# Kernel tuning notes

Hardware: AMD Instinct MI355X
Metric: run time of the kernel (lower is better)

The kernel has to match this reference:

```python
import jax, jax.numpy as jnp
import numpy as np

B, D, S, F, C, H, OUT = 4, 60, 512, 158, 64, 128, 1
LN_EPS = 1e-5


def setup_inputs() -> dict:
    key = jax.random.key(0)
    ks = jax.random.split(key, 12)
    g = lambda k, shape, s=0.05: jax.random.normal(k, shape, dtype=jnp.float32) * s
    return dict(
        x=jax.random.normal(ks[0], (B, D, S, F), dtype=jnp.float32),
        feature_mask=jax.random.randint(ks[1], (B, D, S), 0, 2).astype(bool),
        wq=g(ks[2], (F, C)), bq=jnp.zeros((C,), jnp.float32),
        wk=g(ks[3], (F, C)), bk=jnp.zeros((C,), jnp.float32),
        wv=g(ks[4], (F, C)), bv=jnp.zeros((C,), jnp.float32),
        ln_g=jnp.ones((F + C,), jnp.float32), ln_b=jnp.zeros((F + C,), jnp.float32),
        w_ih=g(ks[5], (3 * H, F + C)), w_hh=g(ks[6], (3 * H, H)),
        b_ih=jnp.zeros((3 * H,), jnp.float32), b_hh=jnp.zeros((3 * H,), jnp.float32),
        w1=g(ks[7], (H, H // 2)), b1=jnp.zeros((H // 2,), jnp.float32),
        w2=g(ks[8], (H // 2, OUT)), b2=jnp.zeros((OUT,), jnp.float32),
    )


def reference(x, feature_mask, wq, bq, wk, bk, wv, bv, ln_g, ln_b,
              w_ih, w_hh, b_ih, b_hh, w1, b1, w2, b2):
    b, d, s, f = x.shape
    c = wq.shape[1]
    h_dim = w_hh.shape[1]

    # --- market context attention, vectorized over (batch, days) ---
    Q = x @ wq + bq            # (B,D,S,C)
    K = x @ wk + bk
    V = x @ wv + bv
    scores = jnp.einsum('bdsc,bdtc->bdst', Q, K) / jnp.sqrt(jnp.float32(c))
    scores = jnp.where(feature_mask[:, :, None, :], scores, -1e9)  # mask keys
    attn = jax.nn.softmax(scores, axis=-1)
    ctx = jnp.einsum('bdst,bdtc->bdsc', attn, V)       # (B,D,S,C)
    ctx = jnp.where(feature_mask[..., None], ctx, 0.0)  # mask queries
    denom = jnp.maximum(feature_mask.sum(axis=2), 1).astype(x.dtype)  # (B,D)
    market = ctx.sum(axis=2) / denom[..., None]         # (B,D,C)

    # --- concat + layernorm ---
    aug = jnp.concatenate(
        [x, jnp.broadcast_to(market[:, :, None, :], (b, d, s, c))], axis=-1)
    mu = aug.mean(-1, keepdims=True)
    var = aug.var(-1, keepdims=True)
    aug = (aug - mu) / jnp.sqrt(var + LN_EPS) * ln_g + ln_b  # (B,D,S,F+C)

    # --- GRU over days, batch = B*S independent sequences ---
    seq = aug.transpose(1, 0, 2, 3).reshape(d, b * s, f + c)  # (D, N, F+C)
    x_proj = seq @ w_ih.T + b_ih                               # (D, N, 3H)

    def step(h, xp):
        hp = h @ w_hh.T + b_hh
        xr, xz, xn = jnp.split(xp, 3, axis=-1)
        hr, hz, hn = jnp.split(hp, 3, axis=-1)
        r = jax.nn.sigmoid(xr + hr)
        z = jax.nn.sigmoid(xz + hz)
        n = jnp.tanh(xn + r * hn)
        return (1.0 - z) * n + z * h, None

    h0 = jnp.zeros((b * s, h_dim), x.dtype)
    h_last, _ = jax.lax.scan(step, h0, x_proj)  # last-step output
    h_last = h_last.reshape(b, s, h_dim)

    # --- output head (dropout inactive in eval) ---
    hid = jax.nn.relu(h_last @ w1 + b1)
    return hid @ w2 + b2  # (B, S, OUT)
```

## Files before the change

kernel.cpp:

```cpp
#include <hip/hip_runtime.h>
#include <hip/hip_bf16.h>
#include <math.h>

#define BB 4
#define DD 60
#define SS 512
#define FF 158
#define CC 64
#define HH 128
#define FC 222
#define G3 384
#define NN 2048
#define BDN 240

#define L2E  1.44269504f
#define L2E2 2.88539008f
#define QSCALE 0.18033688f

typedef _Float16 f16x8 __attribute__((ext_vector_type(8)));
typedef _Float16 f16x4 __attribute__((ext_vector_type(4)));
typedef float f32x4 __attribute__((ext_vector_type(4)));

__device__ __forceinline__ float exp2_hw(float x){ return __builtin_amdgcn_exp2f(x); }
__device__ __forceinline__ float rcp_hw(float x){ return __builtin_amdgcn_rcpf(x); }

__global__ void prep_kernel(const float* __restrict__ w_ih,
                            const float* __restrict__ wq, const float* __restrict__ wk,
                            const float* __restrict__ w_hh,
                            _Float16* __restrict__ wf16, _Float16* __restrict__ wqk,
                            _Float16* __restrict__ whh16, float* __restrict__ Wg){
    int idx = blockIdx.x*256 + threadIdx.x;
    if (idx < BDN*SS) Wg[idx] = 0.0f;
    if (idx < 384*224){
        int n = idx / 224, k = idx % 224;
        float sc = (n < 256) ? L2E : L2E2;
        wf16[idx] = (k < FC) ? (_Float16)(w_ih[n*FC + k] * sc) : (_Float16)0.0f;
    } else if (idx < 384*224 + 128*160){
        int i2 = idx - 384*224;
        int n = i2 / 160, k = i2 % 160;
        float v = 0.0f;
        if (k < FF)
            v = (n < 64) ? wq[k*CC + n] : wk[k*CC + (n-64)];
        wqk[i2] = (_Float16)v;
    } else {
        int i3 = idx - (384*224 + 128*160);
        if (i3 < 384*128){
            int n = i3 / 128;
            float sc = (n < 256) ? L2E : L2E2;
            whh16[i3] = (_Float16)(w_hh[i3] * sc);
        }
    }
}

__global__ __launch_bounds__(256) void qk_kernel(const float* __restrict__ x,
                           const _Float16* __restrict__ wqk,
                           const float* __restrict__ bq, const float* __restrict__ bk,
                           _Float16* __restrict__ Qh, _Float16* __restrict__ Kh){
    __shared__ _Float16 xa[5][64][40];
    int tid  = threadIdx.x;
    int lane = tid & 63, wv = tid >> 6;
    int col  = lane & 15, quad = lane >> 4;
    int row0 = blockIdx.x * 64;

    f16x8 bfr[2][5];
    #pragma unroll
    for (int nt = 0; nt < 2; ++nt){
        int n = wv*32 + nt*16 + col;
        #pragma unroll
        for (int kq = 0; kq < 5; ++kq)
            bfr[nt][kq] = *(const f16x8*)&wqk[n*160 + kq*32 + quad*8];
    }

    if (tid < 128){
        int r = tid >> 1;
        xa[4][r][30 + (tid & 1)] = (_Float16)0.0f;
    }
    {
        const float4* xb4 = (const float4*)(x + (size_t)row0*FF);
        #pragma unroll
        for (int j = 0; j < 10; ++j){
            int i = tid + j*256;
            if (i < 2528){
                float4 v = xb4[i];
                int base = i*4;
                #pragma unroll
                for (int e = 0; e < 4; ++e){
                    int idx = base + e;
                    int r = idx / 158;
                    int k = idx - r*158;
                    xa[k >> 5][r][k & 31] = (_Float16)((&v.x)[e]);
                }
            }
        }
    }
    __syncthreads();

    float bias[2];
    #pragma unroll
    for (int nt = 0; nt < 2; ++nt){
        int n = wv*32 + nt*16 + col;
        bias[nt] = (n < 64) ? bq[n] : bk[n-64];
    }

    #pragma unroll 1
    for (int mt = 0; mt < 4; ++mt){
        f16x8 a[5];
        #pragma unroll
        for (int kq = 0; kq < 5; ++kq)
            a[kq] = *(const f16x8*)&xa[kq][mt*16 + col][quad*8];
        #pragma unroll
        for (int nt = 0; nt < 2; ++nt){
            f32x4 c = {0.0f, 0.0f, 0.0f, 0.0f};
            #pragma unroll
            for (int kq = 0; kq < 5; ++kq)
                c = __builtin_amdgcn_mfma_f32_16x16x32_f16(a[kq], bfr[nt][kq], c, 0, 0, 0);
            int n = wv*32 + nt*16 + col;
            #pragma unroll
            for (int reg = 0; reg < 4; ++reg){
                int row = row0 + mt*16 + quad*4 + reg;
                float val = c[reg] + bias[nt];
                if (n < 64) Qh[(size_t)row*CC + n]      = (_Float16)(val * QSCALE);
                else        Kh[(size_t)row*CC + (n-64)] = (_Float16)val;
            }
        }
    }
}

__global__ __launch_bounds__(512) void attn_kernel(const _Float16* __restrict__ Qh,
                                                   const _Float16* __restrict__ Kh,
                                                   const int* __restrict__ mask,
                                                   float* __restrict__ Wg){
    __shared__ _Float16 kf[2][512][32];
    __shared__ float w_sh[512];
    __shared__ float mk_lds[512];

    int tid  = threadIdx.x;
    int bd   = blockIdx.x >> 1;
    int q0   = (blockIdx.x & 1) * 256;
    int lane = tid & 63, wvw = tid >> 6;
    int col  = lane & 15, quad = lane >> 4;

    const _Float16* qb = Qh + (size_t)(bd*SS)*CC;
    const _Float16* kb = Kh + (size_t)(bd*SS)*CC;

    {
        int t = tid;
        w_sh[t] = 0.0f;
        mk_lds[t] = (mask[bd*SS + t] != 0) ? 1.0f : 0.0f;
    }
    for (int i = tid; i < 4096; i += 512){
        int t = i >> 3, ch = i & 7;
        *(f16x8*)&kf[ch >> 2][t][(ch & 3)*8] = *(const f16x8*)&kb[t*CC + ch*8];
    }

    f16x8 a0[2], a1[2];
    #pragma unroll
    for (int af = 0; af < 2; ++af){
        int row = q0 + wvw*32 + af*16 + col;
        a0[af] = *(const f16x8*)&qb[row*CC + quad*8];
        a1[af] = *(const f16x8*)&qb[row*CC + 32 + quad*8];
    }
    __syncthreads();

    float lacc[2][4] = {{0,0,0,0},{0,0,0,0}};
    #pragma unroll 2
    for (int kt = 0; kt < 32; ++kt){
        f16x8 b0 = *(const f16x8*)&kf[0][kt*16 + col][quad*8];
        f16x8 b1 = *(const f16x8*)&kf[1][kt*16 + col][quad*8];
        float mkv = mk_lds[kt*16 + col];
        #pragma unroll
        for (int af = 0; af < 2; ++af){
            f32x4 c = {0.0f, 0.0f, 0.0f, 0.0f};
            c = __builtin_amdgcn_mfma_f32_16x16x32_f16(a0[af], b0, c, 0, 0, 0);
            c = __builtin_amdgcn_mfma_f32_16x16x32_f16(a1[af], b1, c, 0, 0, 0);
            #pragma unroll
            for (int reg = 0; reg < 4; ++reg)
                lacc[af][reg] += exp2_hw(c[reg]) * mkv;
        }
    }
    float crv[2][4];
    #pragma unroll
    for (int af = 0; af < 2; ++af){
        #pragma unroll
        for (int reg = 0; reg < 4; ++reg){
            float l = lacc[af][reg];
            l += __shfl_xor(l, 1, 64);
            l += __shfl_xor(l, 2, 64);
            l += __shfl_xor(l, 4, 64);
            l += __shfl_xor(l, 8, 64);
            int row = q0 + wvw*32 + af*16 + quad*4 + reg;
            crv[af][reg] = mk_lds[row] * rcp_hw(l);
        }
    }

    #pragma unroll 2
    for (int kt = 0; kt < 32; ++kt){
        f16x8 b0 = *(const f16x8*)&kf[0][kt*16 + col][quad*8];
        f16x8 b1 = *(const f16x8*)&kf[1][kt*16 + col][quad*8];
        float s = 0.0f;
        #pragma unroll
        for (int af = 0; af < 2; ++af){
            f32x4 c = {0.0f, 0.0f, 0.0f, 0.0f};
            c = __builtin_amdgcn_mfma_f32_16x16x32_f16(a0[af], b0, c, 0, 0, 0);
            c = __builtin_amdgcn_mfma_f32_16x16x32_f16(a1[af], b1, c, 0, 0, 0);
            #pragma unroll
            for (int reg = 0; reg < 4; ++reg)
                s = fmaf(exp2_hw(c[reg]), crv[af][reg], s);
        }
        s += __shfl_xor(s, 16, 64);
        s += __shfl_xor(s, 32, 64);
        if (quad == 0)
            atomicAdd(&w_sh[kt*16 + col], s);
    }
    __syncthreads();

    atomicAdd(&Wg[bd*SS + tid], w_sh[tid]);
}

__global__ __launch_bounds__(512) void market_kernel(const float* __restrict__ Wg,
                                                     const int* __restrict__ mask,
                                                     const float* __restrict__ x,
                                                     const float* __restrict__ wv,
                                                     const float* __restrict__ bv,
                                                     float* __restrict__ market){
    __shared__ float wt[512];
    __shared__ float mk[512];
    __shared__ float part[512];

    int tid = threadIdx.x;
    int bd  = blockIdx.x;

    float m_ = (mask[bd*SS + tid] != 0) ? 1.0f : 0.0f;
    mk[tid] = m_;
    wt[tid] = Wg[bd*SS + tid] * m_;
    __syncthreads();

    {
        int tg = tid >> 8;
        int kk = tid & 255;
        float acc = 0.0f;
        if (kk < FF){
            const float* xb = x + ((size_t)bd*SS + tg*256)*FF + kk;
            #pragma unroll 8
            for (int t = 0; t < 256; ++t)
                acc = fmaf(wt[tg*256 + t], xb[(size_t)t*FF], acc);
        }
        part[tg*256 + kk] = acc;
    }
    __syncthreads();
    if (tid < 64){
        int c = tid;
        float m = 0.0f;
        for (int k = 0; k < FF; ++k){
            float y = part[k] + part[256 + k];
            m = fmaf(y, wv[k*CC + c], m);
        }
        float cnt = 0.0f, sw = 0.0f;
        #pragma unroll
        for (int j = 0; j < 8; ++j){
            cnt += mk[c + 64*j];
            sw  += wt[c + 64*j];
        }
        #pragma unroll
        for (int o = 1; o < 64; o <<= 1){
            cnt += __shfl_xor(cnt, o, 64);
            sw  += __shfl_xor(sw,  o, 64);
        }
        market[bd*CC + c] = (m + sw*bv[c]) * rcp_hw(fmaxf(cnt, 1.0f));
    }
}

__global__ __launch_bounds__(512, 2) void xproj_kernel(const float* __restrict__ x,
                             const float* __restrict__ market,
                             const float* __restrict__ ln_g, const float* __restrict__ ln_b,
                             const _Float16* __restrict__ wf16, const float* __restrict__ b_ih,
                             _Float16* __restrict__ XPP){
    __shared__ _Float16 aug[7][64][32];
    int tid  = threadIdx.x;
    int lane = tid & 63, wv = tid >> 6;
    int col  = lane & 15, quad = lane >> 4;
    int row0 = blockIdx.x * 64;

    f16x8 bfr[3][7];
    #pragma unroll
    for (int nt = 0; nt < 3; ++nt){
        int n = wv*48 + nt*16 + col;
        #pragma unroll
        for (int kq = 0; kq < 7; ++kq)
            bfr[nt][kq] = *(const f16x8*)&wf16[n*224 + kq*32 + quad*8];
    }

    {
        int wrow = wv*8 + (lane >> 3);
        int g    = lane & 7;
        int row  = row0 + wrow;
        int d = row / NN, n = row % NN;
        int b = n >> 9, s = n & 511;
        const float* xr = &x[((size_t)((b*DD + d)*SS) + s)*FF];
        const float* mr = &market[(b*DD + d)*CC];
        float v[28];
        float sum = 0.0f, sq = 0.0f;
        #pragma unroll
        for (int j = 0; j < 28; ++j){
            int f = g + 8*j;
            float vv = 0.0f;
            if (f < FF) vv = xr[f];
            else if (f < FC) vv = mr[f - FF];
            v[j] = vv;
            sum += vv; sq += vv*vv;
        }
        sum += __shfl_xor(sum,1,64); sq += __shfl_xor(sq,1,64);
        sum += __shfl_xor(sum,2,64); sq += __shfl_xor(sq,2,64);
        sum += __shfl_xor(sum,4,64); sq += __shfl_xor(sq,4,64);
        float mu   = sum * (1.0f/222.0f);
        float var  = sq * (1.0f/222.0f) - mu*mu;
        float rstd = rsqrtf(var + 1e-5f);
        #pragma unroll
        for (int j = 0; j < 28; ++j){
            int f = g + 8*j;
            float val = (f < FC) ? ((v[j]-mu)*rstd*ln_g[f] + ln_b[f]) : 0.0f;
            aug[f>>5][wrow][f&31] = (_Float16)val;
        }
    }
    __syncthreads();

    float bias[3];
    #pragma unroll
    for (int nt = 0; nt < 3; ++nt){
        int n = wv*48 + nt*16 + col;
        bias[nt] = b_ih[n] * ((n < 256) ? L2E : L2E2);
    }
    const int d    = row0 / NN;
    const int blk0 = (row0 % NN) >> 4;
    #pragma unroll 1
    for (int mt = 0; mt < 4; ++mt){
        f16x8 a[7];
        #pragma unroll
        for (int kq = 0; kq < 7; ++kq)
            a[kq] = *(const f16x8*)&aug[kq][mt*16 + col][quad*8];
        _Float16* obase = XPP + ((size_t)(d*128 + blk0 + mt)*G3) * 16 + quad*4;
        #pragma unroll
        for (int nt = 0; nt < 3; ++nt){
            f32x4 c = {0.0f, 0.0f, 0.0f, 0.0f};
            #pragma unroll
            for (int kq = 0; kq < 7; ++kq)
                c = __builtin_amdgcn_mfma_f32_16x16x32_f16(a[kq], bfr[nt][kq], c, 0, 0, 0);
            int nn = wv*48 + nt*16 + col;
            f16x4 pk;
            pk[0] = (_Float16)(c[0] + bias[nt]);
            pk[1] = (_Float16)(c[1] + bias[nt]);
            pk[2] = (_Float16)(c[2] + bias[nt]);
            pk[3] = (_Float16)(c[3] + bias[nt]);
            *(f16x4*)(obase + (size_t)nn*16) = pk;
        }
    }
}

#define XLOAD(dst, base_) do{                                                   \
    dst[0][0] = *(const f16x4*)((base_));                                       \
    dst[0][1] = *(const f16x4*)((base_) + 128*16);                              \
    dst[0][2] = *(const f16x4*)((base_) + 256*16);                              \
    dst[1][0] = *(const f16x4*)((base_) + 16*16);                               \
    dst[1][1] = *(const f16x4*)((base_) + 144*16);                              \
    dst[1][2] = *(const f16x4*)((base_) + 272*16);                              \
}while(0)

#define BARRIER_NODRAIN() asm volatile("s_waitcnt lgkmcnt(0)\ns_barrier" ::: "memory")

#define GRU_STEP(PRD, PWR, XC, XPF, DOPF) do{                                   \
    if (DOPF && qlow) { XLOAD(XPF, xp_d + 2*DSTR); }                            \
    f16x8 a_[4];                                                                \
    _Pragma("unroll") for (int kq = 0; kq < 4; ++kq)                            \
        a_[kq] = *(const f16x8*)&hfrag[PRD][kq][col][quad*8];                   \
    f32x4 c_[3][2];                                                             \
    _Pragma("unroll") for (int g = 0; g < 3; ++g)                               \
    _Pragma("unroll") for (int hf = 0; hf < 2; ++hf){                           \
        f32x4 acc = {0.0f, 0.0f, 0.0f, 0.0f};                                   \
        _Pragma("unroll") for (int kq = 0; kq < 4; ++kq)                        \
            acc = __builtin_amdgcn_mfma_f32_16x16x32_f16(a_[kq], bfr[g][hf][kq], acc, 0,0,0); \
        c_[g][hf] = acc;                                                        \
    }                                                                           \
    if (qlow){                                                                  \
    _Pragma("unroll") for (int hf = 0; hf < 2; ++hf)                            \
    _Pragma("unroll") for (int rg = 0; rg < 4; ++rg){                           \
        float r_ = rcp_hw(1.0f + exp2_hw(-((float)XC[hf][0][rg] + c_[0][hf][rg] + bh[0][hf]))); \
        float z_ = rcp_hw(1.0f + exp2_hw(-((float)XC[hf][1][rg] + c_[1][hf][rg] + bh[1][hf]))); \
        float e_ = exp2_hw((float)XC[hf][2][rg] + r_*(c_[2][hf][rg] + bh[2][hf])); \
        float n_ = 1.0f - 2.0f*rcp_hw(e_ + 1.0f);                               \
        float h_ = n_ + z_*(hcur[hf][rg] - n_);                                 \
        hcur[hf][rg] = h_;                                                      \
        hfrag[PWR][w][quad*4 + rg][hf*16 + col] = (_Float16)h_;                 \
    }}                                                                          \
    xp_d += DSTR;                                                               \
    BARRIER_NODRAIN();                                                          \
}while(0)

__global__ __launch_bounds__(256, 2) void gru_kernel(const _Float16* __restrict__ XPP,
                                                     const _Float16* __restrict__ whh16,
                                                     const float* __restrict__ b_hh,
                                                     const float* __restrict__ w1, const float* __restrict__ b1,
                                                     const float* __restrict__ w2, const float* __restrict__ b2,
                                                     float* __restrict__ out){
    __shared__ _Float16 hfrag[2][4][16][40];
    __shared__ float h_sh[8][132];

    const int tid  = threadIdx.x;
    const int lane = tid & 63, w = tid >> 6;
    const int col  = lane & 15, quad = lane >> 4;
    const bool qlow = (quad < 2);
    const int row0 = blockIdx.x * 8;

    for (int i = tid; i < 2*4*16*40; i += 256)
        ((_Float16*)hfrag)[i] = (_Float16)0.0f;

    f16x8 bfr[3][2][4];
    #pragma unroll
    for (int g = 0; g < 3; ++g)
    #pragma unroll
    for (int hf = 0; hf < 2; ++hf){
        int n = g*HH + w*32 + hf*16 + col;
        #pragma unroll
        for (int kq = 0; kq < 4; ++kq)
            bfr[g][hf][kq] = *(const f16x8*)&whh16[(size_t)n*HH + kq*32 + quad*8];
    }

    float bh[3][2];
    #pragma unroll
    for (int g = 0; g < 3; ++g)
    #pragma unroll
    for (int hf = 0; hf < 2; ++hf)
        bh[g][hf] = b_hh[g*HH + w*32 + hf*16 + col] * ((g < 2) ? L2E : L2E2);

    const size_t DSTR = (size_t)128 * G3 * 16;
    const _Float16* xp_d = XPP + ((size_t)(blockIdx.x >> 1)*G3 + (w*32 + col))*16
                               + (blockIdx.x & 1)*8 + quad*4;

    f16x4 xA[2][3], xB[2][3], xC[2][3];
    if (qlow){
        XLOAD(xA, xp_d);
        XLOAD(xB, xp_d + DSTR);
    }

    float hcur[2][4] = {{0,0,0,0},{0,0,0,0}};
    __syncthreads();

    #pragma unroll 1
    for (int ch = 0; ch < 10; ++ch){
        const int pf = (ch < 9);
        GRU_STEP(0, 1, xA, xC, 1);
        GRU_STEP(1, 0, xB, xA, 1);
        GRU_STEP(0, 1, xC, xB, 1);
        GRU_STEP(1, 0, xA, xC, 1);
        GRU_STEP(0, 1, xB, xA, pf);
        GRU_STEP(1, 0, xC, xB, pf);
    }

    if (qlow){
        #pragma unroll
        for (int hf = 0; hf < 2; ++hf)
        #pragma unroll
        for (int rg = 0; rg < 4; ++rg)
            h_sh[quad*4 + rg][w*32 + hf*16 + col] = hcur[hf][rg];
    }
    __syncthreads();

    {
        int c2 = tid & 63;
        int rb = tid >> 6;
        #pragma unroll
        for (int rr = 0; rr < 2; ++rr){
            int r = rb + rr*4;
            float acc = 0.0f;
            #pragma unroll 8
            for (int k = 0; k < 128; ++k)
                acc = fmaf(h_sh[r][k], w1[k*64 + c2], acc);
            float hid = fmaxf(acc + b1[c2], 0.0f);
            float o = hid * w2[c2];
            #pragma unroll
            for (int off = 1; off < 64; off <<= 1) o += __shfl_xor(o, off, 64);
            if (c2 == 0) out[row0 + r] = o + b2[0];
        }
    }
}

extern "C" void kernel_launch(void* const* d_in, const int* in_sizes, int n_in,
                              void* d_out, int out_size, void* d_ws, size_t ws_size,
                              hipStream_t stream) {
    const float* x    = (const float*)d_in[0];
    const int*   mask = (const int*)d_in[1];
    const float* wq   = (const float*)d_in[2];
    const float* bq   = (const float*)d_in[3];
    const float* wk   = (const float*)d_in[4];
    const float* bk   = (const float*)d_in[5];
    const float* wv   = (const float*)d_in[6];
    const float* bv   = (const float*)d_in[7];
    const float* ln_g = (const float*)d_in[8];
    const float* ln_b = (const float*)d_in[9];
    const float* w_ih = (const float*)d_in[10];
    const float* w_hh = (const float*)d_in[11];
    const float* b_ih = (const float*)d_in[12];
    const float* b_hh = (const float*)d_in[13];
    const float* w1   = (const float*)d_in[14];
    const float* b1   = (const float*)d_in[15];
    const float* w2   = (const float*)d_in[16];
    const float* b2   = (const float*)d_in[17];

    float* ws = (float*)d_ws;
    _Float16* Qh  = (_Float16*)ws;
    _Float16* Kh  = (_Float16*)(ws + 3932160);
    float*    Wg  = ws + 8000000;
    _Float16* XPP = (_Float16*)ws;
    float* market = ws + 23592960;
    _Float16* wf16 = (_Float16*)(ws + 23608320);
    _Float16* wqk  = (_Float16*)(ws + 23651328);
    _Float16* whh16= (_Float16*)(ws + 23666688);

    prep_kernel<<<648, 256, 0, stream>>>(w_ih, wq, wk, w_hh, wf16, wqk, whh16, Wg);
    qk_kernel<<<1920, 256, 0, stream>>>(x, wqk, bq, bk, Qh, Kh);
    attn_kernel<<<480, 512, 0, stream>>>(Qh, Kh, mask, Wg);
    market_kernel<<<240, 512, 0, stream>>>(Wg, mask, x, wv, bv, market);
    xproj_kernel<<<1920, 512, 0, stream>>>(x, market, ln_g, ln_b, wf16, b_ih, XPP);
    gru_kernel<<<256, 256, 0, stream>>>(XPP, whh16, b_hh, w1, b1, w2, b2, (float*)d_out);
}
```

Baseline: 349.2 us.

## Split GRU across 512 blocks of 4 sequences with 8 waves each

Each GRU block now handles 4 sequences with 512 threads instead of 8 sequences with 256 threads, and each wave owns 16 hidden columns instead of 32. The xproj output layout changes to 4-row blocks so each lane loads one f16x4 per gate. This doubles the grid to 512 blocks so more CUs run the latency-bound sequential recurrence, with less per-thread MFMA and gate work per step. In exchange, 3/4 of each MFMA's rows are padding (only quad 0 is valid), the recurrent weights are replicated across twice as many blocks, and barriers now span 8 waves.

```diff
diff --git a/kernel.cpp b/kernel.cpp
--- a/kernel.cpp
+++ b/kernel.cpp
@@ -330,15 +330,16 @@
         int n = wv*48 + nt*16 + col;
         bias[nt] = b_ih[n] * ((n < 256) ? L2E : L2E2);
     }
-    const int d    = row0 / NN;
-    const int blk0 = (row0 % NN) >> 4;
+    const int d     = row0 / NN;
+    const int rday  = row0 % NN;
     #pragma unroll 1
     for (int mt = 0; mt < 4; ++mt){
         f16x8 a[7];
         #pragma unroll
         for (int kq = 0; kq < 7; ++kq)
             a[kq] = *(const f16x8*)&aug[kq][mt*16 + col][quad*8];
-        _Float16* obase = XPP + ((size_t)(d*128 + blk0 + mt)*G3) * 16 + quad*4;
+        int blk = (rday >> 2) + mt*4 + quad;
+        _Float16* obase = XPP + ((size_t)(d*512 + blk)*G3) * 4;
         #pragma unroll
         for (int nt = 0; nt < 3; ++nt){
             f32x4 c = {0.0f, 0.0f, 0.0f, 0.0f};
@@ -351,97 +352,90 @@
             pk[1] = (_Float16)(c[1] + bias[nt]);
             pk[2] = (_Float16)(c[2] + bias[nt]);
             pk[3] = (_Float16)(c[3] + bias[nt]);
-            *(f16x4*)(obase + (size_t)nn*16) = pk;
-        }
-    }
-}
-
-#define XLOAD(dst, base_) do{                                                   \
-    dst[0][0] = *(const f16x4*)((base_));                                       \
-    dst[0][1] = *(const f16x4*)((base_) + 128*16);                              \
-    dst[0][2] = *(const f16x4*)((base_) + 256*16);                              \
-    dst[1][0] = *(const f16x4*)((base_) + 16*16);                               \
-    dst[1][1] = *(const f16x4*)((base_) + 144*16);                              \
-    dst[1][2] = *(const f16x4*)((base_) + 272*16);                              \
+            *(f16x4*)(obase + (size_t)nn*4) = pk;
+        }
+    }
+}
+
+#define XLOAD4(dst, base_) do{                                                  \
+    dst[0] = *(const f16x4*)((base_));                                          \
+    dst[1] = *(const f16x4*)((base_) + 512);                                    \
+    dst[2] = *(const f16x4*)((base_) + 1024);                                   \
 }while(0)
 
 #define BARRIER_NODRAIN() asm volatile("s_waitcnt lgkmcnt(0)\ns_barrier" ::: "memory")
 
 #define GRU_STEP(PRD, PWR, XC, XPF, DOPF) do{                                   \
-    if (DOPF && qlow) { XLOAD(XPF, xp_d + 2*DSTR); }                            \
+    if (DOPF && qz) { XLOAD4(XPF, xp_d + 2*DSTR); }                             \
     f16x8 a_[4];                                                                \
     _Pragma("unroll") for (int kq = 0; kq < 4; ++kq)                            \
         a_[kq] = *(const f16x8*)&hfrag[PRD][kq][col][quad*8];                   \
-    f32x4 c_[3][2];                                                             \
-    _Pragma("unroll") for (int g = 0; g < 3; ++g)                               \
-    _Pragma("unroll") for (int hf = 0; hf < 2; ++hf){                           \
+    f32x4 c_[3];                                                                \
+    _Pragma("unroll") for (int g = 0; g < 3; ++g){                              \
         f32x4 acc = {0.0f, 0.0f, 0.0f, 0.0f};                                   \
         _Pragma("unroll") for (int kq = 0; kq < 4; ++kq)                        \
-            acc = __builtin_amdgcn_mfma_f32_16x16x32_f16(a_[kq], bfr[g][hf][kq], acc, 0,0,0); \
-        c_[g][hf] = acc;                                                        \
+            acc = __builtin_amdgcn_mfma_f32_16x16x32_f16(a_[kq], bfr[g][kq], acc, 0,0,0); \
+        c_[g] = acc;                                                            \
     }                                                                           \
-    if (qlow){                                                                  \
-    _Pragma("unroll") for (int hf = 0; hf < 2; ++hf)                            \
+    if (qz){                                                                    \
     _Pragma("unroll") for (int rg = 0; rg < 4; ++rg){                           \
-        float r_ = rcp_hw(1.0f + exp2_hw(-((float)XC[hf][0][rg] + c_[0][hf][rg] + bh[0][hf]))); \
-        float z_ = rcp_hw(1.0f + exp2_hw(-((float)XC[hf][1][rg] + c_[1][hf][rg] + bh[1][hf]))); \
-        float e_ = exp2_hw((float)XC[hf][2][rg] + r_*(c_[2][hf][rg] + bh[2][hf])); \
+        float r_ = rcp_hw(1.0f + exp2_hw(-((float)XC[0][rg] + c_[0][rg] + bh0))); \
+        float z_ = rcp_hw(1.0f + exp2_hw(-((float)XC[1][rg] + c_[1][rg] + bh1))); \
+        float e_ = exp2_hw((float)XC[2][rg] + r_*(c_[2][rg] + bh2));            \
         float n_ = 1.0f - 2.0f*rcp_hw(e_ + 1.0f);                               \
-        float h_ = n_ + z_*(hcur[hf][rg] - n_);                                 \
-        hcur[hf][rg] = h_;                                                      \
-        hfrag[PWR][w][quad*4 + rg][hf*16 + col] = (_Float16)h_;                 \
+        float h_ = n_ + z_*(hcur[rg] - n_);                                     \
+        hcur[rg] = h_;                                                          \
+        hfrag[PWR][hkq][rg][hidx] = (_Float16)h_;                               \
     }}                                                                          \
     xp_d += DSTR;                                                               \
     BARRIER_NODRAIN();                                                          \
 }while(0)
 
-__global__ __launch_bounds__(256, 2) void gru_kernel(const _Float16* __restrict__ XPP,
+__global__ __launch_bounds__(512, 4) void gru_kernel(const _Float16* __restrict__ XPP,
                                                      const _Float16* __restrict__ whh16,
                                                      const float* __restrict__ b_hh,
                                                      const float* __restrict__ w1, const float* __restrict__ b1,
                                                      const float* __restrict__ w2, const float* __restrict__ b2,
                                                      float* __restrict__ out){
     __shared__ _Float16 hfrag[2][4][16][40];
-    __shared__ float h_sh[8][132];
+    __shared__ float h_sh[4][132];
 
     const int tid  = threadIdx.x;
     const int lane = tid & 63, w = tid >> 6;
     const int col  = lane & 15, quad = lane >> 4;
-    const bool qlow = (quad < 2);
-    const int row0 = blockIdx.x * 8;
-
-    for (int i = tid; i < 2*4*16*40; i += 256)
+    const bool qz  = (quad == 0);
+    const int row0 = blockIdx.x * 4;
+
+    for (int i = tid; i < 2*4*16*40; i += 512)
         ((_Float16*)hfrag)[i] = (_Float16)0.0f;
 
-    f16x8 bfr[3][2][4];
-    #pragma unroll
-    for (int g = 0; g < 3; ++g)
-    #pragma unroll
-    for (int hf = 0; hf < 2; ++hf){
-        int n = g*HH + w*32 + hf*16 + col;
+    f16x8 bfr[3][4];
+    #pragma unroll
+    for (int g = 0; g < 3; ++g){
+        int n = g*HH + w*16 + col;
         #pragma unroll
         for (int kq = 0; kq < 4; ++kq)
-            bfr[g][hf][kq] = *(const f16x8*)&whh16[(size_t)n*HH + kq*32 + quad*8];
-    }
-
-    float bh[3][2];
-    #pragma unroll
-    for (int g = 0; g < 3; ++g)
-    #pragma unroll
-    for (int hf = 0; hf < 2; ++hf)
-        bh[g][hf] = b_hh[g*HH + w*32 + hf*16 + col] * ((g < 2) ? L2E : L2E2);
-
-    const size_t DSTR = (size_t)128 * G3 * 16;
-    const _Float16* xp_d = XPP + ((size_t)(blockIdx.x >> 1)*G3 + (w*32 + col))*16
-                               + (blockIdx.x & 1)*8 + quad*4;
-
-    f16x4 xA[2][3], xB[2][3], xC[2][3];
-    if (qlow){
-        XLOAD(xA, xp_d);
-        XLOAD(xB, xp_d + DSTR);
-    }
-
-    float hcur[2][4] = {{0,0,0,0},{0,0,0,0}};
+            bfr[g][kq] = *(const f16x8*)&whh16[(size_t)n*HH + kq*32 + quad*8];
+    }
+
+    const float bh0 = b_hh[0*HH + w*16 + col] * L2E;
+    const float bh1 = b_hh[1*HH + w*16 + col] * L2E;
+    const float bh2 = b_hh[2*HH + w*16 + col] * L2E2;
+
+    const int hcol = w*16 + col;
+    const int hkq  = hcol >> 5;
+    const int hidx = hcol & 31;
+
+    const size_t DSTR = (size_t)512 * G3 * 4;
+    const _Float16* xp_d = XPP + ((size_t)blockIdx.x*G3 + hcol)*4;
+
+    f16x4 xA[3], xB[3], xC[3];
+    if (qz){
+        XLOAD4(xA, xp_d);
+        XLOAD4(xB, xp_d + DSTR);
+    }
+
+    float hcur[4] = {0.0f, 0.0f, 0.0f, 0.0f};
     __syncthreads();
 
     #pragma unroll 1
@@ -455,31 +449,25 @@
         GRU_STEP(1, 0, xC, xB, pf);
     }
 
-    if (qlow){
-        #pragma unroll
-        for (int hf = 0; hf < 2; ++hf)
+    if (qz){
         #pragma unroll
         for (int rg = 0; rg < 4; ++rg)
-            h_sh[quad*4 + rg][w*32 + hf*16 + col] = hcur[hf][rg];
-    }
-    __syncthreads();
-
-    {
+            h_sh[rg][hcol] = hcur[rg];
+    }
+    __syncthreads();
+
+    if (tid < 256){
         int c2 = tid & 63;
-        int rb = tid >> 6;
-        #pragma unroll
-        for (int rr = 0; rr < 2; ++rr){
-            int r = rb + rr*4;
-            float acc = 0.0f;
-            #pragma unroll 8
-            for (int k = 0; k < 128; ++k)
-                acc = fmaf(h_sh[r][k], w1[k*64 + c2], acc);
-            float hid = fmaxf(acc + b1[c2], 0.0f);
-            float o = hid * w2[c2];
-            #pragma unroll
-            for (int off = 1; off < 64; off <<= 1) o += __shfl_xor(o, off, 64);
-            if (c2 == 0) out[row0 + r] = o + b2[0];
-        }
+        int r  = tid >> 6;
+        float acc = 0.0f;
+        #pragma unroll 8
+        for (int k = 0; k < 128; ++k)
+            acc = fmaf(h_sh[r][k], w1[k*64 + c2], acc);
+        float hid = fmaxf(acc + b1[c2], 0.0f);
+        float o = hid * w2[c2];
+        #pragma unroll
+        for (int off = 1; off < 64; off <<= 1) o += __shfl_xor(o, off, 64);
+        if (c2 == 0) out[row0 + r] = o + b2[0];
     }
 }
 
@@ -520,5 +508,5 @@
     attn_kernel<<<480, 512, 0, stream>>>(Qh, Kh, mask, Wg);
     market_kernel<<<240, 512, 0, stream>>>(Wg, mask, x, wv, bv, market);
     xproj_kernel<<<1920, 512, 0, stream>>>(x, market, ln_g, ln_b, wf16, b_ih, XPP);
-    gru_kernel<<<256, 256, 0, stream>>>(XPP, whh16, b_hh, w1, b1, w2, b2, (float*)d_out);
-}
+    gru_kernel<<<512, 512, 0, stream>>>(XPP, whh16, b_hh, w1, b1, w2, b2, (float*)d_out);
+}
```

Result: slower. 360.2 us (+3.2%).

## Split market reduction across more blocks and widen GRU blocks to 16 rows

Applied to the files above, without the earlier changes.

The market context reduction is split into two kernels. The first spreads the weighted sum over x across four times as many blocks and combines partial sums with atomics into a zeroed buffer. The second applies wv, bv and the mask count. The GRU kernel now gives each block 16 sequences instead of 8, so all four quads of each wave do useful gate math and the grid is halved to 128 blocks. This means fewer blocks than CUs and one fewer overlapping block per CU, plus an extra kernel launch and atomic traffic.

```diff
diff --git a/kernel.cpp b/kernel.cpp
--- a/kernel.cpp
+++ b/kernel.cpp
@@ -28,9 +28,11 @@
                             const float* __restrict__ wq, const float* __restrict__ wk,
                             const float* __restrict__ w_hh,
                             _Float16* __restrict__ wf16, _Float16* __restrict__ wqk,
-                            _Float16* __restrict__ whh16, float* __restrict__ Wg){
+                            _Float16* __restrict__ whh16, float* __restrict__ Wg,
+                            float* __restrict__ ypart){
     int idx = blockIdx.x*256 + threadIdx.x;
     if (idx < BDN*SS) Wg[idx] = 0.0f;
+    if (idx < BDN*160) ypart[idx] = 0.0f;
     if (idx < 384*224){
         int n = idx / 224, k = idx % 224;
         float sc = (n < 256) ? L2E : L2E2;
@@ -217,22 +219,21 @@
     atomicAdd(&Wg[bd*SS + tid], w_sh[tid]);
 }
 
-__global__ __launch_bounds__(512) void market_kernel(const float* __restrict__ Wg,
-                                                     const int* __restrict__ mask,
-                                                     const float* __restrict__ x,
-                                                     const float* __restrict__ wv,
-                                                     const float* __restrict__ bv,
-                                                     float* __restrict__ market){
-    __shared__ float wt[512];
-    __shared__ float mk[512];
+__global__ __launch_bounds__(512) void market1_kernel(const float* __restrict__ Wg,
+                                                      const int* __restrict__ mask,
+                                                      const float* __restrict__ x,
+                                                      float* __restrict__ ypart){
+    __shared__ float wt[128];
     __shared__ float part[512];
 
     int tid = threadIdx.x;
-    int bd  = blockIdx.x;
-
-    float m_ = (mask[bd*SS + tid] != 0) ? 1.0f : 0.0f;
-    mk[tid] = m_;
-    wt[tid] = Wg[bd*SS + tid] * m_;
+    int bd  = blockIdx.x >> 2;
+    int t0  = (blockIdx.x & 3) * 128;
+
+    if (tid < 128){
+        int t = bd*SS + t0 + tid;
+        wt[tid] = (mask[t] != 0) ? Wg[t] : 0.0f;
+    }
     __syncthreads();
 
     {
@@ -240,34 +241,46 @@
         int kk = tid & 255;
         float acc = 0.0f;
         if (kk < FF){
-            const float* xb = x + ((size_t)bd*SS + tg*256)*FF + kk;
+            const float* xb = x + ((size_t)bd*SS + t0 + tg*64)*FF + kk;
             #pragma unroll 8
-            for (int t = 0; t < 256; ++t)
-                acc = fmaf(wt[tg*256 + t], xb[(size_t)t*FF], acc);
-        }
-        part[tg*256 + kk] = acc;
-    }
-    __syncthreads();
-    if (tid < 64){
-        int c = tid;
-        float m = 0.0f;
-        for (int k = 0; k < FF; ++k){
-            float y = part[k] + part[256 + k];
-            m = fmaf(y, wv[k*CC + c], m);
-        }
-        float cnt = 0.0f, sw = 0.0f;
-        #pragma unroll
-        for (int j = 0; j < 8; ++j){
-            cnt += mk[c + 64*j];
-            sw  += wt[c + 64*j];
-        }
-        #pragma unroll
-        for (int o = 1; o < 64; o <<= 1){
-            cnt += __shfl_xor(cnt, o, 64);
-            sw  += __shfl_xor(sw,  o, 64);
-        }
-        market[bd*CC + c] = (m + sw*bv[c]) * rcp_hw(fmaxf(cnt, 1.0f));
-    }
+            for (int t = 0; t < 64; ++t)
+                acc = fmaf(wt[tg*64 + t], xb[(size_t)t*FF], acc);
+        }
+        part[tid] = acc;
+    }
+    __syncthreads();
+    if (tid < FF)
+        atomicAdd(&ypart[bd*160 + tid], part[tid] + part[256 + tid]);
+}
+
+__global__ __launch_bounds__(64) void market2_kernel(const float* __restrict__ ypart,
+                                                     const float* __restrict__ Wg,
+                                                     const int* __restrict__ mask,
+                                                     const float* __restrict__ wv,
+                                                     const float* __restrict__ bv,
+                                                     float* __restrict__ market){
+    int c  = threadIdx.x;
+    int bd = blockIdx.x;
+
+    const float* y = ypart + bd*160;
+    float m = 0.0f;
+    for (int k = 0; k < FF; ++k)
+        m = fmaf(y[k], wv[k*CC + c], m);
+
+    float cnt = 0.0f, sw = 0.0f;
+    #pragma unroll
+    for (int j = 0; j < 8; ++j){
+        int t = bd*SS + c + 64*j;
+        float mk = (mask[t] != 0) ? 1.0f : 0.0f;
+        cnt += mk;
+        sw  += Wg[t] * mk;
+    }
+    #pragma unroll
+    for (int o = 1; o < 64; o <<= 1){
+        cnt += __shfl_xor(cnt, o, 64);
+        sw  += __shfl_xor(sw,  o, 64);
+    }
+    market[bd*CC + c] = (m + sw*bv[c]) * rcp_hw(fmaxf(cnt, 1.0f));
 }
 
 __global__ __launch_bounds__(512, 2) void xproj_kernel(const float* __restrict__ x,
@@ -368,7 +381,7 @@
 #define BARRIER_NODRAIN() asm volatile("s_waitcnt lgkmcnt(0)\ns_barrier" ::: "memory")
 
 #define GRU_STEP(PRD, PWR, XC, XPF, DOPF) do{                                   \
-    if (DOPF && qlow) { XLOAD(XPF, xp_d + 2*DSTR); }                            \
+    if (DOPF) { XLOAD(XPF, xp_d + 2*DSTR); }                                    \
     f16x8 a_[4];                                                                \
     _Pragma("unroll") for (int kq = 0; kq < 4; ++kq)                            \
         a_[kq] = *(const f16x8*)&hfrag[PRD][kq][col][quad*8];                   \
@@ -380,7 +393,6 @@
             acc = __builtin_amdgcn_mfma_f32_16x16x32_f16(a_[kq], bfr[g][hf][kq], acc, 0,0,0); \
         c_[g][hf] = acc;                                                        \
     }                                                                           \
-    if (qlow){                                                                  \
     _Pragma("unroll") for (int hf = 0; hf < 2; ++hf)                            \
     _Pragma("unroll") for (int rg = 0; rg < 4; ++rg){                           \
         float r_ = rcp_hw(1.0f + exp2_hw(-((float)XC[hf][0][rg] + c_[0][hf][rg] + bh[0][hf]))); \
@@ -390,25 +402,24 @@
         float h_ = n_ + z_*(hcur[hf][rg] - n_);                                 \
         hcur[hf][rg] = h_;                                                      \
         hfrag[PWR][w][quad*4 + rg][hf*16 + col] = (_Float16)h_;                 \
-    }}                                                                          \
+    }                                                                           \
     xp_d += DSTR;                                                               \
     BARRIER_NODRAIN();                                                          \
 }while(0)
 
-__global__ __launch_bounds__(256, 2) void gru_kernel(const _Float16* __restrict__ XPP,
+__global__ __launch_bounds__(256, 1) void gru_kernel(const _Float16* __restrict__ XPP,
                                                      const _Float16* __restrict__ whh16,
                                                      const float* __restrict__ b_hh,
                                                      const float* __restrict__ w1, const float* __restrict__ b1,
                                                      const float* __restrict__ w2, const float* __restrict__ b2,
                                                      float* __restrict__ out){
     __shared__ _Float16 hfrag[2][4][16][40];
-    __shared__ float h_sh[8][132];
+    __shared__ float h_sh[16][132];
 
     const int tid  = threadIdx.x;
     const int lane = tid & 63, w = tid >> 6;
     const int col  = lane & 15, quad = lane >> 4;
-    const bool qlow = (quad < 2);
-    const int row0 = blockIdx.x * 8;
+    const int row0 = blockIdx.x * 16;
 
     for (int i = tid; i < 2*4*16*40; i += 256)
         ((_Float16*)hfrag)[i] = (_Float16)0.0f;
@@ -432,14 +443,11 @@
         bh[g][hf] = b_hh[g*HH + w*32 + hf*16 + col] * ((g < 2) ? L2E : L2E2);
 
     const size_t DSTR = (size_t)128 * G3 * 16;
-    const _Float16* xp_d = XPP + ((size_t)(blockIdx.x >> 1)*G3 + (w*32 + col))*16
-                               + (blockIdx.x & 1)*8 + quad*4;
+    const _Float16* xp_d = XPP + ((size_t)blockIdx.x*G3 + (w*32 + col))*16 + quad*4;
 
     f16x4 xA[2][3], xB[2][3], xC[2][3];
-    if (qlow){
-        XLOAD(xA, xp_d);
-        XLOAD(xB, xp_d + DSTR);
-    }
+    XLOAD(xA, xp_d);
+    XLOAD(xB, xp_d + DSTR);
 
     float hcur[2][4] = {{0,0,0,0},{0,0,0,0}};
     __syncthreads();
@@ -455,21 +463,19 @@
         GRU_STEP(1, 0, xC, xB, pf);
     }
 
-    if (qlow){
-        #pragma unroll
-        for (int hf = 0; hf < 2; ++hf)
-        #pragma unroll
-        for (int rg = 0; rg < 4; ++rg)
-            h_sh[quad*4 + rg][w*32 + hf*16 + col] = hcur[hf][rg];
-    }
+    #pragma unroll
+    for (int hf = 0; hf < 2; ++hf)
+    #pragma unroll
+    for (int rg = 0; rg < 4; ++rg)
+        h_sh[quad*4 + rg][w*32 + hf*16 + col] = hcur[hf][rg];
     __syncthreads();
 
     {
         int c2 = tid & 63;
         int rb = tid >> 6;
         #pragma unroll
-        for (int rr = 0; rr < 2; ++rr){
-            int r = rb + rr*4;
+        for (int rr = 0; rr < 4; ++rr){
+            int r = rb*4 + rr;
             float acc = 0.0f;
             #pragma unroll 8
             for (int k = 0; k < 128; ++k)
@@ -509,16 +515,18 @@
     _Float16* Qh  = (_Float16*)ws;
     _Float16* Kh  = (_Float16*)(ws + 3932160);
     float*    Wg  = ws + 8000000;
+    float*    ypart = ws + 8200000;
     _Float16* XPP = (_Float16*)ws;
     float* market = ws + 23592960;
     _Float16* wf16 = (_Float16*)(ws + 23608320);
     _Float16* wqk  = (_Float16*)(ws + 23651328);
     _Float16* whh16= (_Float16*)(ws + 23666688);
 
-    prep_kernel<<<648, 256, 0, stream>>>(w_ih, wq, wk, w_hh, wf16, wqk, whh16, Wg);
+    prep_kernel<<<648, 256, 0, stream>>>(w_ih, wq, wk, w_hh, wf16, wqk, whh16, Wg, ypart);
     qk_kernel<<<1920, 256, 0, stream>>>(x, wqk, bq, bk, Qh, Kh);
     attn_kernel<<<480, 512, 0, stream>>>(Qh, Kh, mask, Wg);
-    market_kernel<<<240, 512, 0, stream>>>(Wg, mask, x, wv, bv, market);
+    market1_kernel<<<960, 512, 0, stream>>>(Wg, mask, x, ypart);
+    market2_kernel<<<240, 64, 0, stream>>>(ypart, Wg, mask, wv, bv, market);
     xproj_kernel<<<1920, 512, 0, stream>>>(x, market, ln_g, ln_b, wf16, b_ih, XPP);
-    gru_kernel<<<256, 256, 0, stream>>>(XPP, whh16, b_hh, w1, b1, w2, b2, (float*)d_out);
-}
+    gru_kernel<<<128, 256, 0, stream>>>(XPP, whh16, b_hh, w1, b1, w2, b2, (float*)d_out);
+}
```

After: 350.1 us. About the same (+0.3%).
